# Performance work log

Measured on AMD Instinct MI355X. Metric: run time of the kernel, lower is better.

The kernel has to match this reference:

```python
import jax, jax.numpy as jnp
import numpy as np

B, N, D, E = 2, 50000, 128, 800000
EPS = 1e-5


def layer_norm(x, gamma, beta):
    m = jnp.mean(x, axis=-1, keepdims=True)
    v = jnp.mean((x - m) ** 2, axis=-1, keepdims=True)
    return (x - m) * jax.lax.rsqrt(v + EPS) * gamma + beta


def setup_inputs() -> dict:
    key = jax.random.key(0)
    ks = jax.random.split(key, 8)
    x = jax.random.normal(ks[0], (B, N, D), dtype=jnp.float32)
    edge_src = jax.random.randint(ks[1], (E,), 0, N)
    edge_dst = jax.random.randint(ks[2], (E,), 0, N)
    # degree consistent with edge_dst (in-degree), as a float tensor
    degree = jax.ops.segment_sum(jnp.ones((E,), jnp.float32), edge_dst, num_segments=N)
    # LayerNorm params (torch default init: gamma=1, beta=0)
    sn_g = jnp.ones((D,), jnp.float32); sn_b = jnp.zeros((D,), jnp.float32)
    nn_g = jnp.ones((D,), jnp.float32); nn_b = jnp.zeros((D,), jnp.float32)
    # MLP: Linear(2D, 2D) -> GELU -> Linear(2D, D); stored as [in, out]
    s1 = 1.0 / np.sqrt(2 * D)
    W1 = jax.random.uniform(ks[3], (2 * D, 2 * D), jnp.float32, -s1, s1)
    b1 = jax.random.uniform(ks[4], (2 * D,), jnp.float32, -s1, s1)
    W2 = jax.random.uniform(ks[5], (2 * D, D), jnp.float32, -s1, s1)
    b2 = jax.random.uniform(ks[6], (D,), jnp.float32, -s1, s1)
    return {"x": x, "edge_src": edge_src, "edge_dst": edge_dst, "degree": degree,
            "sn_g": sn_g, "sn_b": sn_b, "nn_g": nn_g, "nn_b": nn_b,
            "W1": W1, "b1": b1, "W2": W2, "b2": b2}


def reference(x, edge_src, edge_dst, degree, sn_g, sn_b, nn_g, nn_b, W1, b1, W2, b2):
    # gather messages from source nodes, scatter-add into destination nodes
    neighbor = jnp.zeros_like(x).at[:, edge_dst, :].add(x[:, edge_src, :])  # [B,N,D]
    neighbor = neighbor / jnp.clip(degree, 1.0)[None, :, None]
    h = jnp.concatenate([layer_norm(x, sn_g, sn_b), layer_norm(neighbor, nn_g, nn_b)], axis=-1)  # [B,N,2D]
    h = jax.nn.gelu(h @ W1 + b1, approximate=False)  # torch nn.GELU default = exact erf
    return x + (h @ W2 + b2)
```

## Files before the change

### kernel.cpp

```cpp
#include <hip/hip_runtime.h>
#include <cstdint>

#define B_ 2
#define N_ 50000
#define D_ 128
#define E_ 800000
#define TOK 100000

typedef __bf16 bf16x8 __attribute__((ext_vector_type(8)));
typedef float f32x4 __attribute__((ext_vector_type(4)));

__device__ __forceinline__ unsigned short f2bf(float f) {
  union { float f; uint32_t u; } v; v.f = f;
  uint32_t u = v.u;
  return (unsigned short)((u + 0x7FFFu + ((u >> 16) & 1u)) >> 16);
}
__device__ __forceinline__ float uasf(uint32_t u) {
  union { uint32_t u; float f; } v; v.u = u; return v.f;
}
__device__ __forceinline__ float fast_gelu(float v) {
  float p = v * (1.5957691f + 0.07135481f * v * v);
  return v * __builtin_amdgcn_rcpf(1.0f + __expf(-p));
}

__global__ __launch_bounds__(256) void prep_k(
    const float* __restrict__ x, const float* __restrict__ W1,
    const float* __restrict__ W2, const int* __restrict__ edst,
    unsigned short* __restrict__ xb, unsigned short* __restrict__ W1t,
    unsigned short* __restrict__ W2t, int* __restrict__ cnt) {
  const int blk = blockIdx.x;
  if (blk < 12500) {
    int q = (blk * 256 + threadIdx.x) * 4;
    int node = q >> 8;
    int rem = q & 255;
    int b = rem >> 7, c = rem & 127;
    float4 v = *(const float4*)(x + (size_t)b * (N_ * D_) + node * 128 + c);
    uint2 p = { (uint32_t)f2bf(v.x) | ((uint32_t)f2bf(v.y) << 16),
                (uint32_t)f2bf(v.z) | ((uint32_t)f2bf(v.w) << 16) };
    *(uint2*)(xb + q) = p;
  } else if (blk < 12884) {
    int t = (blk - 12500) * 256 + threadIdx.x;
    if (t < 65536) {
      int n = t >> 8, k = t & 255;
      int f = (n >> 4) * 8 + (k >> 5);
      int pos = ((n & 15) + ((k >> 3) & 3) * 16) * 8 + (k & 7);
      W1t[f * 512 + pos] = f2bf(W1[k * 256 + n]);
    } else {
      int t2 = t - 65536;
      int n = t2 >> 8, k = t2 & 255;
      int f = (n >> 4) * 8 + (k >> 5);
      int pos = ((n & 15) + ((k >> 3) & 3) * 16) * 8 + (k & 7);
      W2t[f * 512 + pos] = f2bf(W2[k * 128 + n]);
    }
  } else {
    int e = (blk - 12884) * 256 + threadIdx.x;
    if (e < E_) atomicAdd(&cnt[edst[e]], 1);
  }
}

__global__ __launch_bounds__(1024) void scan_all_k(const int* __restrict__ cnt,
                                                   int* __restrict__ rs,
                                                   int* __restrict__ cursor) {
  __shared__ int wsum[16], woff[16], carry[2];
  const int tid = threadIdx.x, lane = tid & 63, wv = tid >> 6;
  if (tid == 0) carry[0] = 0;
  int p = 0;
  __syncthreads();
  for (int base = 0; base < N_; base += 4096) {
    int i = base + tid * 4;
    int4 v = {0, 0, 0, 0};
    if (i + 3 < N_) {
      v = *(const int4*)(cnt + i);
    } else {
      if (i     < N_) v.x = cnt[i];
      if (i + 1 < N_) v.y = cnt[i + 1];
      if (i + 2 < N_) v.z = cnt[i + 2];
      if (i + 3 < N_) v.w = cnt[i + 3];
    }
    int s4 = v.x + v.y + v.z + v.w;
    int s = s4;
#pragma unroll
    for (int off = 1; off < 64; off <<= 1) {
      int t = __shfl_up(s, off);
      if (lane >= off) s += t;
    }
    if (lane == 63) wsum[wv] = s;
    __syncthreads();
    if (tid == 0) {
      int a = 0;
#pragma unroll
      for (int w = 0; w < 16; ++w) { woff[w] = a; a += wsum[w]; }
      carry[p ^ 1] = carry[p] + a;
    }
    __syncthreads();
    int pre = carry[p] + woff[wv] + (s - s4);
    int e0 = pre, e1 = pre + v.x, e2 = e1 + v.y, e3 = e2 + v.z;
    if (i + 3 < N_) {
      int4 w0 = {e0, e1, e2, e3};
      *(int4*)(rs + i) = w0;
      *(int4*)(cursor + i) = w0;
    } else {
      if (i     < N_) { rs[i]     = e0; cursor[i]     = e0; }
      if (i + 1 < N_) { rs[i + 1] = e1; cursor[i + 1] = e1; }
      if (i + 2 < N_) { rs[i + 2] = e2; cursor[i + 2] = e2; }
      if (i + 3 < N_) { rs[i + 3] = e3; cursor[i + 3] = e3; }
    }
    p ^= 1;
  }
  if (tid == 0) rs[N_] = E_;
}

__global__ __launch_bounds__(256) void fill_k(const int* __restrict__ esrc,
                                              const int* __restrict__ edst,
                                              int* __restrict__ cursor,
                                              int* __restrict__ sorted_src) {
  int e4 = (blockIdx.x * 256 + threadIdx.x) * 4;
  if (e4 < E_) {
    int4 s4 = *(const int4*)(esrc + e4);
    int4 d4 = *(const int4*)(edst + e4);
    int p0 = atomicAdd(&cursor[d4.x], 1); sorted_src[p0] = s4.x;
    int p1 = atomicAdd(&cursor[d4.y], 1); sorted_src[p1] = s4.y;
    int p2 = atomicAdd(&cursor[d4.z], 1); sorted_src[p2] = s4.z;
    int p3 = atomicAdd(&cursor[d4.w], 1); sorted_src[p3] = s4.w;
  }
}

__global__ __launch_bounds__(256) void gather_ln_k(
    const unsigned short* __restrict__ xb,
    const int* __restrict__ rs, const int* __restrict__ ss,
    const float* __restrict__ sn_g, const float* __restrict__ sn_b,
    const float* __restrict__ nn_g, const float* __restrict__ nn_b,
    unsigned short* __restrict__ h) {
  const int node = blockIdx.x * 4 + (threadIdx.x >> 6);
  const int lane = threadIdx.x & 63;
  const int g = lane >> 5;
  const int l32 = lane & 31;
  const int r0 = rs[node], r1 = rs[node + 1];
  const unsigned short* xrow = xb + l32 * 8;
  float acc[8] = {0.f, 0.f, 0.f, 0.f, 0.f, 0.f, 0.f, 0.f};
  for (int e = r0; e < r1; e += 16) {
    int idx[8];
#pragma unroll
    for (int j = 0; j < 8; ++j) {
      int ej = e + 2 * j + g;
      idx[j] = ss[(ej < r1) ? ej : r0];
    }
    uint4 v[8];
#pragma unroll
    for (int j = 0; j < 8; ++j)
      v[j] = *(const uint4*)(xrow + (size_t)idx[j] * 256);
#pragma unroll
    for (int j = 0; j < 8; ++j) {
      if (e + 2 * j + g < r1) {
        acc[0] += uasf(v[j].x << 16); acc[1] += uasf(v[j].x & 0xffff0000u);
        acc[2] += uasf(v[j].y << 16); acc[3] += uasf(v[j].y & 0xffff0000u);
        acc[4] += uasf(v[j].z << 16); acc[5] += uasf(v[j].z & 0xffff0000u);
        acc[6] += uasf(v[j].w << 16); acc[7] += uasf(v[j].w & 0xffff0000u);
      }
    }
  }
#pragma unroll
  for (int k = 0; k < 8; ++k) acc[k] += __shfl_xor(acc[k], 32);
  const float invd = 1.0f / fmaxf((float)(r1 - r0), 1.0f);
  float nb[8];
#pragma unroll
  for (int k = 0; k < 8; ++k) nb[k] = acc[k] * invd;
  uint4 xq = *(const uint4*)(xrow + (size_t)node * 256);
  float xv[8];
  xv[0] = uasf(xq.x << 16); xv[1] = uasf(xq.x & 0xffff0000u);
  xv[2] = uasf(xq.y << 16); xv[3] = uasf(xq.y & 0xffff0000u);
  xv[4] = uasf(xq.z << 16); xv[5] = uasf(xq.z & 0xffff0000u);
  xv[6] = uasf(xq.w << 16); xv[7] = uasf(xq.w & 0xffff0000u);
  float sx = 0.f, sxx = 0.f, sn = 0.f, snn = 0.f;
#pragma unroll
  for (int k = 0; k < 8; ++k) {
    sx += xv[k]; sxx += xv[k] * xv[k];
    sn += nb[k]; snn += nb[k] * nb[k];
  }
#pragma unroll
  for (int off = 1; off < 16; off <<= 1) {
    sx  += __shfl_xor(sx, off);  sxx += __shfl_xor(sxx, off);
    sn  += __shfl_xor(sn, off);  snn += __shfl_xor(snn, off);
  }
  const float r = 1.0f / 128.0f;
  float mx = sx * r, vx = fmaxf(sxx * r - mx * mx, 0.f);
  float mn = sn * r, vn = fmaxf(snn * r - mn * mn, 0.f);
  float rx = rsqrtf(vx + 1e-5f), rn = rsqrtf(vn + 1e-5f);
  const int c = (l32 & 15) * 8;
  const float* gp = g ? nn_g : sn_g;
  const float* bp = g ? nn_b : sn_b;
  float4 g0 = *(const float4*)(gp + c), g1 = *(const float4*)(gp + c + 4);
  float4 b0 = *(const float4*)(bp + c), b1v = *(const float4*)(bp + c + 4);
  float gw[8] = {g0.x, g0.y, g0.z, g0.w, g1.x, g1.y, g1.z, g1.w};
  float bw[8] = {b0.x, b0.y, b0.z, b0.w, b1v.x, b1v.y, b1v.z, b1v.w};
  float mu = g ? mn : mx;
  float rs_ = g ? rn : rx;
  float o[8];
#pragma unroll
  for (int k = 0; k < 8; ++k) {
    float s = g ? nb[k] : xv[k];
    o[k] = (s - mu) * rs_ * gw[k] + bw[k];
  }
  uint4 po;
  po.x = (uint32_t)f2bf(o[0]) | ((uint32_t)f2bf(o[1]) << 16);
  po.y = (uint32_t)f2bf(o[2]) | ((uint32_t)f2bf(o[3]) << 16);
  po.z = (uint32_t)f2bf(o[4]) | ((uint32_t)f2bf(o[5]) << 16);
  po.w = (uint32_t)f2bf(o[6]) | ((uint32_t)f2bf(o[7]) << 16);
  unsigned short* hr = h + ((size_t)(l32 >> 4) * N_ + node) * 256 + g * 128 + c;
  *(uint4*)hr = po;
}

__global__ __launch_bounds__(256, 4) void fused_mlp_k(
    const unsigned short* __restrict__ A,
    const unsigned short* __restrict__ W1t,
    const unsigned short* __restrict__ W2t,
    const float* __restrict__ b1,
    const float* __restrict__ b2,
    const float* __restrict__ resid,
    float* __restrict__ outp, int M) {
  __shared__ unsigned short As[64 * 256];
  __shared__ unsigned short Hc[64 * 64];
  const int tid = threadIdx.x;
  const int wave = tid >> 6, lane = tid & 63;
  const int wr = wave >> 1;
  const int wc = wave & 1;
  const int quad = lane >> 4, l15 = lane & 15;
  const int m0 = blockIdx.x * 64;
  {
    uint4 v[8];
#pragma unroll
    for (int it = 0; it < 8; ++it) {
      int id = it * 256 + tid;
      int r = id >> 5, c16 = id & 31;
      int gm = m0 + r;
      uint4 va = {0u, 0u, 0u, 0u};
      if (gm < M) va = *(const uint4*)(A + (size_t)gm * 256 + c16 * 8);
      v[it] = va;
    }
#pragma unroll
    for (int it = 0; it < 8; ++it) {
      int id = it * 256 + tid;
      int r = id >> 5, c16 = id & 31;
      *(uint4*)(&As[r * 256 + (c16 ^ (r & 7)) * 8]) = v[it];
    }
  }
  f32x4 acc2[2][4] = {};
  __syncthreads();
  for (int nc = 0; nc < 4; ++nc) {
    f32x4 acc1[2][2] = {};
#pragma unroll
    for (int kc = 0; kc < 256; kc += 32) {
      bf16x8 a[2], b[2];
#pragma unroll
      for (int i = 0; i < 2; ++i) {
        int row = wr * 32 + i * 16 + l15;
        a[i] = *(const bf16x8*)(&As[row * 256 + ((kc + quad * 8) ^ ((row & 7) << 3))]);
      }
#pragma unroll
      for (int i = 0; i < 2; ++i) {
        int ftile = (nc * 4 + wc * 2 + i) * 8 + (kc >> 5);
        b[i] = *(const bf16x8*)(W1t + ftile * 512 + lane * 8);
      }
#pragma unroll
      for (int mi = 0; mi < 2; ++mi)
#pragma unroll
        for (int ni = 0; ni < 2; ++ni)
          acc1[mi][ni] = __builtin_amdgcn_mfma_f32_16x16x32_bf16(a[mi], b[ni], acc1[mi][ni], 0, 0, 0);
    }
    __syncthreads();
#pragma unroll
    for (int mi = 0; mi < 2; ++mi)
#pragma unroll
      for (int ni = 0; ni < 2; ++ni) {
        int col = wc * 32 + ni * 16 + l15;
        float bv = b1[nc * 64 + col];
#pragma unroll
        for (int rr = 0; rr < 4; ++rr) {
          int row = wr * 32 + mi * 16 + quad * 4 + rr;
          Hc[row * 64 + (col ^ ((row & 7) << 3))] = f2bf(fast_gelu(acc1[mi][ni][rr] + bv));
        }
      }
    __syncthreads();
#pragma unroll
    for (int kc = 0; kc < 64; kc += 32) {
      bf16x8 a[2], b[4];
#pragma unroll
      for (int i = 0; i < 2; ++i) {
        int row = wr * 32 + i * 16 + l15;
        a[i] = *(const bf16x8*)(&Hc[row * 64 + ((kc + quad * 8) ^ ((row & 7) << 3))]);
      }
#pragma unroll
      for (int i = 0; i < 4; ++i) {
        int ftile = (wc * 4 + i) * 8 + nc * 2 + (kc >> 5);
        b[i] = *(const bf16x8*)(W2t + ftile * 512 + lane * 8);
      }
#pragma unroll
      for (int mi = 0; mi < 2; ++mi)
#pragma unroll
        for (int ni = 0; ni < 4; ++ni)
          acc2[mi][ni] = __builtin_amdgcn_mfma_f32_16x16x32_bf16(a[mi], b[ni], acc2[mi][ni], 0, 0, 0);
    }
  }
#pragma unroll
  for (int mi = 0; mi < 2; ++mi)
#pragma unroll
    for (int ni = 0; ni < 4; ++ni) {
      int col = wc * 64 + ni * 16 + l15;
      float bv = b2[col];
#pragma unroll
      for (int rr = 0; rr < 4; ++rr) {
        int row = m0 + wr * 32 + mi * 16 + quad * 4 + rr;
        if (row < M) {
          float v = acc2[mi][ni][rr] + bv + resid[(size_t)row * 128 + col];
          outp[(size_t)row * 128 + col] = v;
        }
      }
    }
}

extern "C" void kernel_launch(void* const* d_in, const int* in_sizes, int n_in,
                              void* d_out, int out_size, void* d_ws, size_t ws_size,
                              hipStream_t stream) {
  const float* x    = (const float*)d_in[0];
  const int* esrc   = (const int*)d_in[1];
  const int* edst   = (const int*)d_in[2];
  const float* sn_g = (const float*)d_in[4];
  const float* sn_b = (const float*)d_in[5];
  const float* nn_g = (const float*)d_in[6];
  const float* nn_b = (const float*)d_in[7];
  const float* W1   = (const float*)d_in[8];
  const float* b1   = (const float*)d_in[9];
  const float* W2   = (const float*)d_in[10];
  const float* b2   = (const float*)d_in[11];

  char* ws = (char*)d_ws;
  const size_t H_BYTES = (size_t)TOK * 256 * 2;
  unsigned short* h = (unsigned short*)ws;
  char* csr = ws + H_BYTES;
  int* cnt        = (int*)(csr);
  int* rs         = (int*)(csr + 400000);
  int* cursor     = (int*)(csr + 600016);
  int* sorted_src = (int*)(csr + 800512);
  unsigned short* xb = (unsigned short*)(csr + 4194304);
  unsigned short* W1t = (unsigned short*)(ws + 2 * H_BYTES);
  unsigned short* W2t = W1t + 65536;

  hipMemsetAsync(cnt, 0, (size_t)N_ * sizeof(int), stream);
  prep_k<<<16009, 256, 0, stream>>>(x, W1, W2, edst, xb, W1t, W2t, cnt);
  scan_all_k<<<1, 1024, 0, stream>>>(cnt, rs, cursor);
  fill_k<<<(E_ / 4 + 255) / 256, 256, 0, stream>>>(esrc, edst, cursor, sorted_src);
  gather_ln_k<<<N_ / 4, 256, 0, stream>>>(xb, rs, sorted_src,
                                          sn_g, sn_b, nn_g, nn_b, h);
  fused_mlp_k<<<(TOK + 63) / 64, 256, 0, stream>>>(h, W1t, W2t, b1, b2,
                                                   x, (float*)d_out, TOK);
}
```

Baseline: 336.3 us.

## Replace per-node atomic CSR fill with two-pass bucketed counting sort

The CSR fill now runs in two passes. First, edges are scattered into 64-node buckets using one global atomic cursor per bucket, and each entry packs the source index with the low bits of its destination. Second, one block per bucket redistributes its entries to exact node positions using shared-memory atomics. This aims to cut the cost of scattered global atomics on 50000 per-node cursors. In exchange it adds a kernel launch and a pass over a temp buffer, and bucket-level atomics are more heavily contended. The 16-bit packing assumes source indices stay below 65536.

```diff
diff --git a/kernel.cpp b/kernel.cpp
--- a/kernel.cpp
+++ b/kernel.cpp
@@ -6,6 +6,7 @@
 #define D_ 128
 #define E_ 800000
 #define TOK 100000
+#define NBUCK 782
 
 typedef __bf16 bf16x8 __attribute__((ext_vector_type(8)));
 typedef float f32x4 __attribute__((ext_vector_type(4)));
@@ -60,7 +61,7 @@
 
 __global__ __launch_bounds__(1024) void scan_all_k(const int* __restrict__ cnt,
                                                    int* __restrict__ rs,
-                                                   int* __restrict__ cursor) {
+                                                   int* __restrict__ bcur) {
   __shared__ int wsum[16], woff[16], carry[2];
   const int tid = threadIdx.x, lane = tid & 63, wv = tid >> 6;
   if (tid == 0) carry[0] = 0;
@@ -95,33 +96,55 @@
     __syncthreads();
     int pre = carry[p] + woff[wv] + (s - s4);
     int e0 = pre, e1 = pre + v.x, e2 = e1 + v.y, e3 = e2 + v.z;
+    if (i < N_ && (i & 63) == 0) bcur[i >> 6] = e0;
     if (i + 3 < N_) {
       int4 w0 = {e0, e1, e2, e3};
       *(int4*)(rs + i) = w0;
-      *(int4*)(cursor + i) = w0;
     } else {
-      if (i     < N_) { rs[i]     = e0; cursor[i]     = e0; }
-      if (i + 1 < N_) { rs[i + 1] = e1; cursor[i + 1] = e1; }
-      if (i + 2 < N_) { rs[i + 2] = e2; cursor[i + 2] = e2; }
-      if (i + 3 < N_) { rs[i + 3] = e3; cursor[i + 3] = e3; }
+      if (i     < N_) rs[i]     = e0;
+      if (i + 1 < N_) rs[i + 1] = e1;
+      if (i + 2 < N_) rs[i + 2] = e2;
+      if (i + 3 < N_) rs[i + 3] = e3;
     }
     p ^= 1;
   }
   if (tid == 0) rs[N_] = E_;
 }
 
-__global__ __launch_bounds__(256) void fill_k(const int* __restrict__ esrc,
-                                              const int* __restrict__ edst,
-                                              int* __restrict__ cursor,
-                                              int* __restrict__ sorted_src) {
+__global__ __launch_bounds__(256) void fill_a_k(const int* __restrict__ esrc,
+                                                const int* __restrict__ edst,
+                                                int* __restrict__ bcur,
+                                                int* __restrict__ tmp) {
   int e4 = (blockIdx.x * 256 + threadIdx.x) * 4;
   if (e4 < E_) {
     int4 s4 = *(const int4*)(esrc + e4);
     int4 d4 = *(const int4*)(edst + e4);
-    int p0 = atomicAdd(&cursor[d4.x], 1); sorted_src[p0] = s4.x;
-    int p1 = atomicAdd(&cursor[d4.y], 1); sorted_src[p1] = s4.y;
-    int p2 = atomicAdd(&cursor[d4.z], 1); sorted_src[p2] = s4.z;
-    int p3 = atomicAdd(&cursor[d4.w], 1); sorted_src[p3] = s4.w;
+    int p0 = atomicAdd(&bcur[d4.x >> 6], 1); tmp[p0] = s4.x | ((d4.x & 63) << 16);
+    int p1 = atomicAdd(&bcur[d4.y >> 6], 1); tmp[p1] = s4.y | ((d4.y & 63) << 16);
+    int p2 = atomicAdd(&bcur[d4.z >> 6], 1); tmp[p2] = s4.z | ((d4.z & 63) << 16);
+    int p3 = atomicAdd(&bcur[d4.w >> 6], 1); tmp[p3] = s4.w | ((d4.w & 63) << 16);
+  }
+}
+
+__global__ __launch_bounds__(256) void fill_b_k(const int* __restrict__ rs,
+                                                const int* __restrict__ tmp,
+                                                int* __restrict__ sorted_src) {
+  __shared__ int cur[64];
+  const int b = blockIdx.x;
+  const int base = b * 64;
+  if (threadIdx.x < 64) {
+    int d = base + threadIdx.x;
+    cur[threadIdx.x] = rs[(d < N_) ? d : N_];
+  }
+  __syncthreads();
+  const int start = rs[base];
+  const int endd  = rs[(base + 64 < N_) ? base + 64 : N_];
+  for (int i = start + threadIdx.x; i < endd; i += 256) {
+    int v = tmp[i];
+    int src = v & 0xFFFF;
+    int d6 = (v >> 16) & 63;
+    int p = atomicAdd(&cur[d6], 1);
+    sorted_src[p] = src;
   }
 }
 
@@ -336,10 +359,11 @@
   char* ws = (char*)d_ws;
   const size_t H_BYTES = (size_t)TOK * 256 * 2;
   unsigned short* h = (unsigned short*)ws;
+  int* tmp = (int*)ws;
   char* csr = ws + H_BYTES;
   int* cnt        = (int*)(csr);
   int* rs         = (int*)(csr + 400000);
-  int* cursor     = (int*)(csr + 600016);
+  int* bcur       = (int*)(csr + 600016);
   int* sorted_src = (int*)(csr + 800512);
   unsigned short* xb = (unsigned short*)(csr + 4194304);
   unsigned short* W1t = (unsigned short*)(ws + 2 * H_BYTES);
@@ -347,8 +371,9 @@
 
   hipMemsetAsync(cnt, 0, (size_t)N_ * sizeof(int), stream);
   prep_k<<<16009, 256, 0, stream>>>(x, W1, W2, edst, xb, W1t, W2t, cnt);
-  scan_all_k<<<1, 1024, 0, stream>>>(cnt, rs, cursor);
-  fill_k<<<(E_ / 4 + 255) / 256, 256, 0, stream>>>(esrc, edst, cursor, sorted_src);
+  scan_all_k<<<1, 1024, 0, stream>>>(cnt, rs, bcur);
+  fill_a_k<<<(E_ / 4 + 255) / 256, 256, 0, stream>>>(esrc, edst, bcur, tmp);
+  fill_b_k<<<NBUCK, 256, 0, stream>>>(rs, tmp, sorted_src);
   gather_ln_k<<<N_ / 4, 256, 0, stream>>>(xb, rs, sorted_src,
                                           sn_g, sn_b, nn_g, nn_b, h);
   fused_mlp_k<<<(TOK + 63) / 64, 256, 0, stream>>>(h, W1t, W2t, b1, b2,
```

New measurement: 480.5 us. +42.9%, slower.
